# Kernel tuning notes

Measured on AMD Instinct MI355X. Metric: run time of the kernel, lower is better.

Reference implementation:

```python
import jax, jax.numpy as jnp
import numpy as np

N_NODES = 100000
N_EDGES = 500000
D_IN = 128
D_HID = 128
D_OUT = 128


def _sage_conv(x, src, dst, W_l, b_l, W_r, n_nodes):
    # mean aggregation of source-node features at destination nodes
    msg = jax.ops.segment_sum(x[src], dst, num_segments=n_nodes)          # [N, d_in]
    cnt = jax.ops.segment_sum(jnp.ones((src.shape[0], 1), x.dtype), dst,
                              num_segments=n_nodes)                        # [N, 1]
    agg = msg / jnp.maximum(cnt, 1.0)
    # PyG SAGEConv: lin_l(aggregated) + lin_r(self), bias on lin_l only
    return agg @ W_l + b_l + x @ W_r


def setup_inputs() -> dict:
    key = jax.random.key(0)
    ks = jax.random.split(key, 8)
    x = jax.random.normal(ks[0], (N_NODES, D_IN), dtype=jnp.float32)
    edge_index = jax.random.randint(ks[1], (2, N_EDGES), 0, N_NODES, dtype=jnp.int32)
    s1 = 1.0 / np.sqrt(D_IN)
    s2 = 1.0 / np.sqrt(D_HID)
    W_l1 = jax.random.uniform(ks[2], (D_IN, D_HID), jnp.float32, -s1, s1)
    W_r1 = jax.random.uniform(ks[3], (D_IN, D_HID), jnp.float32, -s1, s1)
    b_l1 = jnp.zeros((D_HID,), jnp.float32)
    W_l2 = jax.random.uniform(ks[4], (D_HID, D_OUT), jnp.float32, -s2, s2)
    W_r2 = jax.random.uniform(ks[5], (D_HID, D_OUT), jnp.float32, -s2, s2)
    b_l2 = jnp.zeros((D_OUT,), jnp.float32)
    return {"x": x, "edge_index": edge_index,
            "W_l1": W_l1, "b_l1": b_l1, "W_r1": W_r1,
            "W_l2": W_l2, "b_l2": b_l2, "W_r2": W_r2}


def reference(x, edge_index, W_l1, b_l1, W_r1, W_l2, b_l2, W_r2):
    src, dst = edge_index[0], edge_index[1]
    h = _sage_conv(x, src, dst, W_l1, b_l1, W_r1, N_NODES)
    h = jax.nn.relu(h)
    out = _sage_conv(h, src, dst, W_l2, b_l2, W_r2, N_NODES)
    return out
```

## Files before the change

kernel.cpp:

```cpp
#include <hip/hip_runtime.h>
#include <cstddef>

#define N_NODES 100000
#define N_EDGES 500000
#define D 128

typedef __attribute__((ext_vector_type(8))) short bf16x8;
typedef __attribute__((ext_vector_type(4))) float f32x4;

static __device__ __forceinline__ short f2bf(float f)
{
    unsigned u = __builtin_bit_cast(unsigned, f);
    unsigned r = (u + 0x7fffu + ((u >> 16) & 1u)) >> 16;
    return (short)r;
}
static __device__ __forceinline__ float b2f(short s)
{
    return __builtin_bit_cast(float, (unsigned)((unsigned short)s) << 16);
}


__global__ __launch_bounds__(256)
void hist_kernel(const int* __restrict__ dst, int* __restrict__ deg)
{
    int e = blockIdx.x * 256 + threadIdx.x;
    if (e < N_EDGES) atomicAdd(&deg[dst[e]], 1);
}

__global__ __launch_bounds__(512)
void scanA_kernel(const int* __restrict__ deg, int* __restrict__ bsum)
{
    __shared__ int s[512];
    int t = threadIdx.x;
    int idx = blockIdx.x * 512 + t;
    s[t] = (idx < N_NODES) ? deg[idx] : 0;
    __syncthreads();
    for (int off = 256; off > 0; off >>= 1) {
        if (t < off) s[t] += s[t + off];
        __syncthreads();
    }
    if (t == 0) bsum[blockIdx.x] = s[0];
}

__global__ __launch_bounds__(256)
void scanB_kernel(const int* __restrict__ bsum, int* __restrict__ boff)
{
    __shared__ int s[256];
    int t = threadIdx.x;
    int v = (t < 196) ? bsum[t] : 0;
    s[t] = v;
    __syncthreads();
    for (int off = 1; off < 256; off <<= 1) {
        int a = s[t];
        if (t >= off) a += s[t - off];
        __syncthreads();
        s[t] = a;
        __syncthreads();
    }
    if (t < 196) boff[t] = s[t] - v;
}

__global__ __launch_bounds__(512)
void scanC_kernel(const int* __restrict__ deg, const int* __restrict__ boff,
                  int* __restrict__ row_ptr, int* __restrict__ cursor)
{
    __shared__ int s[512];
    int t = threadIdx.x;
    int idx = blockIdx.x * 512 + t;
    int v = (idx < N_NODES) ? deg[idx] : 0;
    s[t] = v;
    __syncthreads();
    for (int off = 1; off < 512; off <<= 1) {
        int a = s[t];
        if (t >= off) a += s[t - off];
        __syncthreads();
        s[t] = a;
        __syncthreads();
    }
    int excl = boff[blockIdx.x] + s[t] - v;
    if (idx < N_NODES) { row_ptr[idx] = excl; cursor[idx] = excl; }
    else if (idx == N_NODES) { row_ptr[idx] = excl; }
}

__global__ __launch_bounds__(256)
void permute_kernel(const int* __restrict__ src, const int* __restrict__ dst,
                    int* __restrict__ cursor, int* __restrict__ perm)
{
    int e = blockIdx.x * 256 + threadIdx.x;
    if (e < N_EDGES) {
        int pos = atomicAdd(&cursor[dst[e]], 1);
        perm[pos] = src[e];
    }
}

__global__ __launch_bounds__(256)
void cast_kernel(const float* __restrict__ in, short* __restrict__ outb)
{
    int i = blockIdx.x * 256 + threadIdx.x;
    const float4* p = reinterpret_cast<const float4*>(in) + (size_t)i * 2;
    float4 lo = p[0], hi = p[1];
    bf16x8 v;
    v[0] = f2bf(lo.x); v[1] = f2bf(lo.y); v[2] = f2bf(lo.z); v[3] = f2bf(lo.w);
    v[4] = f2bf(hi.x); v[5] = f2bf(hi.y); v[6] = f2bf(hi.z); v[7] = f2bf(hi.w);
    *reinterpret_cast<bf16x8*>(outb + (size_t)i * 8) = v;
}

__global__ __launch_bounds__(256)
void gather_kernel(const short* __restrict__ xb,
                   const int* __restrict__ row_ptr,
                   const int* __restrict__ perm,
                   short* __restrict__ aggb)
{
    unsigned gid = blockIdx.x * 256 + threadIdx.x;
    unsigned node = gid >> 4;
    unsigned c8 = (gid & 15) << 3;
    if (node >= N_NODES) return;
    int beg = row_ptr[node];
    int end = row_ptr[node + 1];
    float acc[8] = {};
    int e = beg;
    for (; e + 2 <= end; e += 2) {
        int s0 = perm[e], s1 = perm[e + 1];
        bf16x8 v0 = *reinterpret_cast<const bf16x8*>(xb + (size_t)s0 * D + c8);
        bf16x8 v1 = *reinterpret_cast<const bf16x8*>(xb + (size_t)s1 * D + c8);
        #pragma unroll
        for (int j = 0; j < 8; ++j) acc[j] += b2f(v0[j]) + b2f(v1[j]);
    }
    if (e < end) {
        int s0 = perm[e];
        bf16x8 v0 = *reinterpret_cast<const bf16x8*>(xb + (size_t)s0 * D + c8);
        #pragma unroll
        for (int j = 0; j < 8; ++j) acc[j] += b2f(v0[j]);
    }
    float inv = 1.0f / fmaxf((float)(end - beg), 1.0f);
    bf16x8 o;
    #pragma unroll
    for (int j = 0; j < 8; ++j) o[j] = f2bf(acc[j] * inv);
    *reinterpret_cast<bf16x8*>(aggb + (size_t)node * D + c8) = o;
}

__global__ __launch_bounds__(256)
void pack_w_kernel(const float* __restrict__ Wl1, const float* __restrict__ Wr1,
                   const float* __restrict__ Wl2, const float* __restrict__ Wr2,
                   short* __restrict__ blob)
{
    int tid = blockIdx.x * 256 + threadIdx.x;
    if (tid >= 8192) return;
    int lane = tid & 63;
    int frag = (tid >> 6) & 63;
    int layer = tid >> 12;
    int cb = frag & 7;
    int ks = frag >> 3;
    int k0 = ks * 32 + (lane >> 4) * 8;
    int col = cb * 16 + (lane & 15);
    const float* Wl = layer ? Wl2 : Wl1;
    const float* Wr = layer ? Wr2 : Wr1;
    const float* W = (k0 < 128) ? (Wl + (size_t)k0 * D) : (Wr + (size_t)(k0 - 128) * D);
    bf16x8 v;
    #pragma unroll
    for (int j = 0; j < 8; ++j)
        v[j] = f2bf(W[(size_t)j * D + col]);
    *reinterpret_cast<bf16x8*>(blob + (size_t)tid * 8) = v;
}

__global__ __launch_bounds__(256)
void mfma_gemm_kernel(const short* __restrict__ aggb,
                      const short* __restrict__ selfb,
                      const short* __restrict__ blob,
                      const float* __restrict__ bias,
                      float* __restrict__ outf,
                      short* __restrict__ outb,
                      int mode)
{
    const int tid = threadIdx.x;
    const int w = tid >> 6;
    const int lane = tid & 63;
    const int kch = lane >> 4;
    int row = blockIdx.x * 64 + w * 16 + (lane & 15);
    int rowc = row < N_NODES ? row : N_NODES - 1;

    const short* aggp = aggb + (size_t)rowc * D + kch * 8;
    const short* selfp = selfb + (size_t)rowc * D + kch * 8;

    f32x4 acc[8] = {};

    #pragma unroll
    for (int ks = 0; ks < 8; ++ks) {
        const short* src = (ks < 4) ? (aggp + ks * 32) : (selfp + (ks - 4) * 32);
        bf16x8 a = *reinterpret_cast<const bf16x8*>(src);
        const short* bptr = blob + ((size_t)(ks * 8) * 64 + lane) * 8;
        #pragma unroll
        for (int cb = 0; cb < 8; ++cb) {
            bf16x8 b = *reinterpret_cast<const bf16x8*>(bptr + (size_t)cb * 64 * 8);
            acc[cb] = __builtin_amdgcn_mfma_f32_16x16x32_bf16(a, b, acc[cb], 0, 0, 0);
        }
    }

    const int colg = lane & 15;
    const int rbase = blockIdx.x * 64 + w * 16 + (lane >> 4) * 4;
    #pragma unroll
    for (int cb = 0; cb < 8; ++cb) {
        int col = cb * 16 + colg;
        float bv = bias[col];
        #pragma unroll
        for (int r = 0; r < 4; ++r) {
            int rr = rbase + r;
            if (rr < N_NODES) {
                float v = acc[cb][r] + bv;
                if (mode) {
                    v = fmaxf(v, 0.0f);
                    outb[(size_t)rr * D + col] = f2bf(v);
                } else {
                    outf[(size_t)rr * D + col] = v;
                }
            }
        }
    }
}

extern "C" void kernel_launch(void* const* d_in, const int* in_sizes, int n_in,
                              void* d_out, int out_size, void* d_ws, size_t ws_size,
                              hipStream_t stream)
{
    const float* x   = (const float*)d_in[0];
    const int*   ei  = (const int*)d_in[1];
    const int*   src = ei;
    const int*   dst = ei + N_EDGES;
    const float* Wl1 = (const float*)d_in[2];
    const float* bl1 = (const float*)d_in[3];
    const float* Wr1 = (const float*)d_in[4];
    const float* Wl2 = (const float*)d_in[5];
    const float* bl2 = (const float*)d_in[6];
    const float* Wr2 = (const float*)d_in[7];
    float* out = (float*)d_out;

    int* deg     = (int*)d_ws;
    int* row_ptr = deg + N_NODES;
    int* cursor  = row_ptr + N_NODES + 1;
    int* bsum    = cursor + N_NODES;
    int* boff    = bsum + 256;
    int* perm    = boff + 256;
    size_t int_end = (size_t)(3 * N_NODES + 1 + 512) + N_EDGES;
    int_end = (int_end + 3) & ~(size_t)3;
    short* blob1 = (short*)((int*)d_ws + int_end);
    short* blob2 = blob1 + 32768;
    short* xb    = blob2 + 32768;
    short* aggb  = xb + (size_t)N_NODES * D;

    const int edge_blocks = (N_EDGES + 255) / 256;
    const int scan_blocks = (N_NODES + 512) / 512;
    const int cast_blocks = (N_NODES * D / 8) / 256;
    const int gath_blocks = (N_NODES * 16) / 256;
    const int gemm_blocks = (N_NODES + 63) / 64;

    hipMemsetAsync(deg, 0, N_NODES * sizeof(int), stream);
    hist_kernel<<<edge_blocks, 256, 0, stream>>>(dst, deg);
    scanA_kernel<<<scan_blocks, 512, 0, stream>>>(deg, bsum);
    scanB_kernel<<<1, 256, 0, stream>>>(bsum, boff);
    scanC_kernel<<<scan_blocks, 512, 0, stream>>>(deg, boff, row_ptr, cursor);
    permute_kernel<<<edge_blocks, 256, 0, stream>>>(src, dst, cursor, perm);
    cast_kernel<<<cast_blocks, 256, 0, stream>>>(x, xb);
    pack_w_kernel<<<32, 256, 0, stream>>>(Wl1, Wr1, Wl2, Wr2, blob1);

    gather_kernel<<<gath_blocks, 256, 0, stream>>>(xb, row_ptr, perm, aggb);
    mfma_gemm_kernel<<<gemm_blocks, 256, 0, stream>>>(aggb, xb, blob1, bl1,
                                                      nullptr, xb, 1);

    gather_kernel<<<gath_blocks, 256, 0, stream>>>(xb, row_ptr, perm, aggb);
    mfma_gemm_kernel<<<gemm_blocks, 256, 0, stream>>>(aggb, xb, blob2, bl2,
                                                      out, nullptr, 0);
}
```

Before: 296.1 us.

## Fuse neighbor mean-gather into MFMA GEMM via swizzled shared-memory tile

Merges the gather kernel and the GEMM kernel of each SAGE layer into one kernel. Each block gathers and averages neighbor features for its 64 rows into an XOR-swizzled LDS tile, then runs the MFMA GEMM reading the aggregated half from LDS. This removes the aggregated intermediate's round trip through global memory and two launches. Layer 1 now writes to a separate buffer so layer 2 can gather from it without read/write hazards. The trade-offs are 16 KB of LDS per block and a fused kernel that mixes latency-bound gathers with the GEMM, which may lower occupancy.

```diff
diff --git a/kernel.cpp b/kernel.cpp
--- a/kernel.cpp
+++ b/kernel.cpp
@@ -103,40 +103,6 @@
     v[0] = f2bf(lo.x); v[1] = f2bf(lo.y); v[2] = f2bf(lo.z); v[3] = f2bf(lo.w);
     v[4] = f2bf(hi.x); v[5] = f2bf(hi.y); v[6] = f2bf(hi.z); v[7] = f2bf(hi.w);
     *reinterpret_cast<bf16x8*>(outb + (size_t)i * 8) = v;
-}
-
-__global__ __launch_bounds__(256)
-void gather_kernel(const short* __restrict__ xb,
-                   const int* __restrict__ row_ptr,
-                   const int* __restrict__ perm,
-                   short* __restrict__ aggb)
-{
-    unsigned gid = blockIdx.x * 256 + threadIdx.x;
-    unsigned node = gid >> 4;
-    unsigned c8 = (gid & 15) << 3;
-    if (node >= N_NODES) return;
-    int beg = row_ptr[node];
-    int end = row_ptr[node + 1];
-    float acc[8] = {};
-    int e = beg;
-    for (; e + 2 <= end; e += 2) {
-        int s0 = perm[e], s1 = perm[e + 1];
-        bf16x8 v0 = *reinterpret_cast<const bf16x8*>(xb + (size_t)s0 * D + c8);
-        bf16x8 v1 = *reinterpret_cast<const bf16x8*>(xb + (size_t)s1 * D + c8);
-        #pragma unroll
-        for (int j = 0; j < 8; ++j) acc[j] += b2f(v0[j]) + b2f(v1[j]);
-    }
-    if (e < end) {
-        int s0 = perm[e];
-        bf16x8 v0 = *reinterpret_cast<const bf16x8*>(xb + (size_t)s0 * D + c8);
-        #pragma unroll
-        for (int j = 0; j < 8; ++j) acc[j] += b2f(v0[j]);
-    }
-    float inv = 1.0f / fmaxf((float)(end - beg), 1.0f);
-    bf16x8 o;
-    #pragma unroll
-    for (int j = 0; j < 8; ++j) o[j] = f2bf(acc[j] * inv);
-    *reinterpret_cast<bf16x8*>(aggb + (size_t)node * D + c8) = o;
 }
 
 __global__ __launch_bounds__(256)
@@ -164,30 +130,75 @@
 }
 
 __global__ __launch_bounds__(256)
-void mfma_gemm_kernel(const short* __restrict__ aggb,
-                      const short* __restrict__ selfb,
-                      const short* __restrict__ blob,
-                      const float* __restrict__ bias,
-                      float* __restrict__ outf,
-                      short* __restrict__ outb,
-                      int mode)
-{
+void fused_layer_kernel(const short* __restrict__ gsrc,
+                        const short* __restrict__ selfb,
+                        const int* __restrict__ row_ptr,
+                        const int* __restrict__ perm,
+                        const short* __restrict__ blob,
+                        const float* __restrict__ bias,
+                        float* __restrict__ outf,
+                        short* __restrict__ outb,
+                        int mode)
+{
+    __shared__ short As[64 * 128];
+
     const int tid = threadIdx.x;
+    const int row0 = blockIdx.x * 64;
+
+    {
+        const int c8 = (tid & 15) * 8;
+        for (int p = 0; p < 4; ++p) {
+            int r = p * 16 + (tid >> 4);
+            int node = row0 + r;
+            if (node < N_NODES) {
+                int beg = row_ptr[node];
+                int end = row_ptr[node + 1];
+                float acc[8] = {};
+                int e = beg;
+                for (; e + 2 <= end; e += 2) {
+                    int s0 = perm[e], s1 = perm[e + 1];
+                    bf16x8 v0 = *reinterpret_cast<const bf16x8*>(gsrc + (size_t)s0 * D + c8);
+                    bf16x8 v1 = *reinterpret_cast<const bf16x8*>(gsrc + (size_t)s1 * D + c8);
+                    #pragma unroll
+                    for (int j = 0; j < 8; ++j) acc[j] += b2f(v0[j]) + b2f(v1[j]);
+                }
+                if (e < end) {
+                    int s0 = perm[e];
+                    bf16x8 v0 = *reinterpret_cast<const bf16x8*>(gsrc + (size_t)s0 * D + c8);
+                    #pragma unroll
+                    for (int j = 0; j < 8; ++j) acc[j] += b2f(v0[j]);
+                }
+                float inv = 1.0f / fmaxf((float)(end - beg), 1.0f);
+                bf16x8 o;
+                #pragma unroll
+                for (int j = 0; j < 8; ++j) o[j] = f2bf(acc[j] * inv);
+                int idx = (r * 128 + c8) ^ ((r & 7) << 3);
+                *reinterpret_cast<bf16x8*>(As + idx) = o;
+            }
+        }
+    }
+    __syncthreads();
+
     const int w = tid >> 6;
     const int lane = tid & 63;
     const int kch = lane >> 4;
-    int row = blockIdx.x * 64 + w * 16 + (lane & 15);
+    const int rloc = w * 16 + (lane & 15);
+    int row = row0 + rloc;
     int rowc = row < N_NODES ? row : N_NODES - 1;
 
-    const short* aggp = aggb + (size_t)rowc * D + kch * 8;
     const short* selfp = selfb + (size_t)rowc * D + kch * 8;
 
     f32x4 acc[8] = {};
 
     #pragma unroll
     for (int ks = 0; ks < 8; ++ks) {
-        const short* src = (ks < 4) ? (aggp + ks * 32) : (selfp + (ks - 4) * 32);
-        bf16x8 a = *reinterpret_cast<const bf16x8*>(src);
+        bf16x8 a;
+        if (ks < 4) {
+            int idx = (rloc * 128 + ks * 32 + kch * 8) ^ ((rloc & 7) << 3);
+            a = *reinterpret_cast<const bf16x8*>(As + idx);
+        } else {
+            a = *reinterpret_cast<const bf16x8*>(selfp + (ks - 4) * 32);
+        }
         const short* bptr = blob + ((size_t)(ks * 8) * 64 + lane) * 8;
         #pragma unroll
         for (int cb = 0; cb < 8; ++cb) {
@@ -197,7 +208,7 @@
     }
 
     const int colg = lane & 15;
-    const int rbase = blockIdx.x * 64 + w * 16 + (lane >> 4) * 4;
+    const int rbase = row0 + w * 16 + (lane >> 4) * 4;
     #pragma unroll
     for (int cb = 0; cb < 8; ++cb) {
         int col = cb * 16 + colg;
@@ -245,13 +256,12 @@
     short* blob1 = (short*)((int*)d_ws + int_end);
     short* blob2 = blob1 + 32768;
     short* xb    = blob2 + 32768;
-    short* aggb  = xb + (size_t)N_NODES * D;
+    short* hb    = xb + (size_t)N_NODES * D;
 
     const int edge_blocks = (N_EDGES + 255) / 256;
     const int scan_blocks = (N_NODES + 512) / 512;
     const int cast_blocks = (N_NODES * D / 8) / 256;
-    const int gath_blocks = (N_NODES * 16) / 256;
-    const int gemm_blocks = (N_NODES + 63) / 64;
+    const int fuse_blocks = (N_NODES + 63) / 64;
 
     hipMemsetAsync(deg, 0, N_NODES * sizeof(int), stream);
     hist_kernel<<<edge_blocks, 256, 0, stream>>>(dst, deg);
@@ -262,11 +272,9 @@
     cast_kernel<<<cast_blocks, 256, 0, stream>>>(x, xb);
     pack_w_kernel<<<32, 256, 0, stream>>>(Wl1, Wr1, Wl2, Wr2, blob1);
 
-    gather_kernel<<<gath_blocks, 256, 0, stream>>>(xb, row_ptr, perm, aggb);
-    mfma_gemm_kernel<<<gemm_blocks, 256, 0, stream>>>(aggb, xb, blob1, bl1,
-                                                      nullptr, xb, 1);
-
-    gather_kernel<<<gath_blocks, 256, 0, stream>>>(xb, row_ptr, perm, aggb);
-    mfma_gemm_kernel<<<gemm_blocks, 256, 0, stream>>>(aggb, xb, blob2, bl2,
-                                                      out, nullptr, 0);
-}
+    fused_layer_kernel<<<fuse_blocks, 256, 0, stream>>>(xb, xb, row_ptr, perm,
+                                                        blob1, bl1, nullptr, hb, 1);
+
+    fused_layer_kernel<<<fuse_blocks, 256, 0, stream>>>(hb, hb, row_ptr, perm,
+                                                        blob2, bl2, out, nullptr, 0);
+}
```

Result: no change. 293.4 us (-0.9%).
